# Performance work log

Measured on AMD Instinct MI355X. Metric: run time of the kernel, lower is better.

The kernel has to match this reference:

```python
import jax, jax.numpy as jnp
import numpy as np

EPS = 1e-8  # torch CosineSimilarity eps


def _l2_normalize(x):
    n = jnp.sqrt(jnp.sum(x * x, axis=-1, keepdims=True))
    return x / jnp.maximum(n, EPS)


def setup_inputs() -> dict:
    key = jax.random.key(0)
    k1, k2, k3 = jax.random.split(key, 3)
    B, D, K = 4096, 1024, 256
    datapoints = jax.random.normal(k1, (B, D), dtype=jnp.float32)
    centroid = jax.random.normal(k2, (K, D), dtype=jnp.float32)
    batch_cos_sim = jax.random.normal(k3, (B, B), dtype=jnp.float32)
    return {"datapoints": datapoints, "centroid": centroid, "batch_cos_sim": batch_cos_sim}


def reference(datapoints, centroid, batch_cos_sim):
    # --- _clustering: cosine similarity datapoints[B,D] vs centroid[K,D] (temp=1) ---
    dn = _l2_normalize(datapoints)                       # [B, D]
    cn = _l2_normalize(centroid)                         # [K, D]
    intra_cos_sim = jnp.einsum('bd,kd->bk', dn, cn)      # [B, K]
    dp_index = jnp.argmax(intra_cos_sim, axis=-1)        # [B]

    # --- _intra_class_adjacency: one-hot matmul, zero diagonal ---
    onehot = jax.nn.one_hot(dp_index, centroid.shape[0], dtype=jnp.float32)  # [B, K]
    dp_cluster = jnp.einsum('bk,ck->bc', onehot, onehot)                      # [B, B]
    B = datapoints.shape[0]
    dp_cluster = dp_cluster * (1.0 - jnp.eye(B, dtype=dp_cluster.dtype))
    index_dp = onehot.T.astype(jnp.int32)                # [K, B]

    # --- gather centroid each datapoint belongs to ---
    dp_centroid = centroid[dp_index]                     # [B, D]

    # --- provide_hard_negative: top-2, take 2nd-best centroid ---
    top_vals, top_idx = jax.lax.top_k(intra_cos_sim, 2)  # [B, 2]
    hard_neg_index = top_idx[:, 1]                       # [B]
    hard_negative = centroid[hard_neg_index]             # [B, D]

    return (intra_cos_sim, dp_index, dp_cluster, index_dp, dp_centroid,
            hard_negative, hard_neg_index, top_vals[:, 1])
```

## Files before the change

### kernel.cpp

```cpp
#include <hip/hip_runtime.h>
#include <hip/hip_bf16.h>
#include <math.h>

#define B_N 4096
#define D_N 1024
#define K_N 256
#define BK 32
#define NSTEP (D_N / BK)

typedef __attribute__((ext_vector_type(8))) short bf16x8;
typedef __attribute__((ext_vector_type(8))) unsigned short u16x8;
typedef __attribute__((ext_vector_type(4))) float f32x4;

static constexpr float K_EPS = 1e-8f;

static __device__ __forceinline__ unsigned short f32_to_bf16_rne(float f) {
    unsigned x = __builtin_bit_cast(unsigned, f);
    unsigned r = (x + 0x7FFFu + ((x >> 16) & 1u)) >> 16;
    return (unsigned short)r;
}
static __device__ __forceinline__ float bf16_bits_to_f32(unsigned short h) {
    unsigned x = ((unsigned)h) << 16;
    return __builtin_bit_cast(float, x);
}

__global__ __launch_bounds__(256) void kcent_kernel(
    const float* __restrict__ cent,
    ushort* __restrict__ phi, ushort* __restrict__ plo)
{
    int n   = blockIdx.x;
    int tid = threadIdx.x;
    float4 v = reinterpret_cast<const float4*>(cent + (size_t)n * D_N)[tid];
    float s = v.x * v.x + v.y * v.y + v.z * v.z + v.w * v.w;
    #pragma unroll
    for (int o = 32; o > 0; o >>= 1) s += __shfl_down(s, o);
    __shared__ float red[4];
    __shared__ float s_inv;
    if ((tid & 63) == 0) red[tid >> 6] = s;
    __syncthreads();
    if (tid == 0) {
        float t = red[0] + red[1] + red[2] + red[3];
        s_inv = 1.0f / fmaxf(sqrtf(t), K_EPS);
    }
    __syncthreads();
    float inv = s_inv;
    float e[4] = {v.x * inv, v.y * inv, v.z * inv, v.w * inv};
    ushort h4[4], l4[4];
    #pragma unroll
    for (int j = 0; j < 4; ++j) {
        ushort h = f32_to_bf16_rne(e[j]);
        float lo = e[j] - bf16_bits_to_f32(h);
        h4[j] = h;
        l4[j] = f32_to_bf16_rne(lo);
    }
    int nt = n >> 4, lr = n & 15;
    int k8 = tid >> 1, half = tid & 1;
    int t  = k8 >> 2, lg = k8 & 3;
    size_t chunk = (size_t)(nt * 32 + t) * 64 + lg * 16 + lr;
    *reinterpret_cast<ushort4*>(phi + chunk * 8 + half * 4) =
        make_ushort4(h4[0], h4[1], h4[2], h4[3]);
    *reinterpret_cast<ushort4*>(plo + chunk * 8 + half * 4) =
        make_ushort4(l4[0], l4[1], l4[2], l4[3]);
}

__global__ __launch_bounds__(512, 4) void kmain_kernel(
    const float* __restrict__ dp, const float* __restrict__ cent,
    const ushort* __restrict__ phi, const ushort* __restrict__ plo,
    float* __restrict__ out_sims, float* __restrict__ out_dpidx,
    float* __restrict__ out_hnidx, float* __restrict__ out_top1,
    float* __restrict__ out_dpcent, float* __restrict__ out_hneg,
    int* __restrict__ ws_dpidx)
{
    __shared__ ushort AhL[16 * 1024];
    __shared__ ushort AlL[16 * 1024];
    __shared__ float  simsL[16 * 256];
    int tid  = threadIdx.x;
    int lane = tid & 63;
    int w    = tid >> 6;
    int lr   = lane & 15;
    int lg   = lane >> 4;
    int brow = blockIdx.x * 16;

    {
        int grp = tid & 31;
        int row = tid >> 5;
        const float4* r4 = reinterpret_cast<const float4*>(
            dp + (size_t)(brow + row) * D_N);
        float s = 0.f;
        #pragma unroll
        for (int q = 0; q < 4; ++q) {
            float4 a = r4[grp * 2 + q * 64];
            float4 b = r4[grp * 2 + 1 + q * 64];
            s += a.x*a.x + a.y*a.y + a.z*a.z + a.w*a.w;
            s += b.x*b.x + b.y*b.y + b.z*b.z + b.w*b.w;
        }
        #pragma unroll
        for (int o = 1; o < 32; o <<= 1) s += __shfl_xor(s, o);
        float inv = 1.0f / fmaxf(sqrtf(s), K_EPS);
        asm volatile("" ::: "memory");
        #pragma unroll
        for (int q = 0; q < 4; ++q) {
            float4 a = r4[grp * 2 + q * 64];
            float4 b = r4[grp * 2 + 1 + q * 64];
            float e0 = a.x*inv, e1 = a.y*inv, e2 = a.z*inv, e3 = a.w*inv;
            float e4 = b.x*inv, e5 = b.y*inv, e6 = b.z*inv, e7 = b.w*inv;
            ushort h0=f32_to_bf16_rne(e0), h1=f32_to_bf16_rne(e1),
                   h2=f32_to_bf16_rne(e2), h3=f32_to_bf16_rne(e3),
                   h4=f32_to_bf16_rne(e4), h5=f32_to_bf16_rne(e5),
                   h6=f32_to_bf16_rne(e6), h7=f32_to_bf16_rne(e7);
            u16x8 hv = {h0,h1,h2,h3,h4,h5,h6,h7};
            u16x8 lv = {f32_to_bf16_rne(e0 - bf16_bits_to_f32(h0)),
                        f32_to_bf16_rne(e1 - bf16_bits_to_f32(h1)),
                        f32_to_bf16_rne(e2 - bf16_bits_to_f32(h2)),
                        f32_to_bf16_rne(e3 - bf16_bits_to_f32(h3)),
                        f32_to_bf16_rne(e4 - bf16_bits_to_f32(h4)),
                        f32_to_bf16_rne(e5 - bf16_bits_to_f32(h5)),
                        f32_to_bf16_rne(e6 - bf16_bits_to_f32(h6)),
                        f32_to_bf16_rne(e7 - bf16_bits_to_f32(h7))};
            int slot = (q * 32 + grp) ^ (row & 7);
            *reinterpret_cast<u16x8*>(&AhL[row * 1024 + slot * 8]) = hv;
            *reinterpret_cast<u16x8*>(&AlL[row * 1024 + slot * 8]) = lv;
        }
    }
    __syncthreads();

    const ushort* bh0 = phi + (size_t)w * 32768 + lane * 8;
    const ushort* bl0 = plo + (size_t)w * 32768 + lane * 8;
    const ushort* bh1 = bh0 + 16384;
    const ushort* bl1 = bl0 + 16384;

    f32x4 acc[2] = {};
    const char* AhC = (const char*)AhL;
    const char* AlC = (const char*)AlL;

    auto step = [&](int t, bf16x8 h0, bf16x8 l0, bf16x8 h1, bf16x8 l1) {
        int g = 4 * t + lg;
        unsigned ca = (unsigned)(g ^ (lr & 7));
        unsigned ao = (unsigned)lr * 2048u + ca * 16u;
        bf16x8 ah = *reinterpret_cast<const bf16x8*>(AhC + ao);
        bf16x8 al = *reinterpret_cast<const bf16x8*>(AlC + ao);
        acc[0] = __builtin_amdgcn_mfma_f32_16x16x32_bf16(ah, h0, acc[0], 0, 0, 0);
        acc[0] = __builtin_amdgcn_mfma_f32_16x16x32_bf16(ah, l0, acc[0], 0, 0, 0);
        acc[0] = __builtin_amdgcn_mfma_f32_16x16x32_bf16(al, h0, acc[0], 0, 0, 0);
        acc[1] = __builtin_amdgcn_mfma_f32_16x16x32_bf16(ah, h1, acc[1], 0, 0, 0);
        acc[1] = __builtin_amdgcn_mfma_f32_16x16x32_bf16(ah, l1, acc[1], 0, 0, 0);
        acc[1] = __builtin_amdgcn_mfma_f32_16x16x32_bf16(al, h1, acc[1], 0, 0, 0);
    };

    #define LB(t, H0, L0, H1, L1)                                        \
        H0 = *reinterpret_cast<const bf16x8*>(bh0 + (t) * 512);          \
        L0 = *reinterpret_cast<const bf16x8*>(bl0 + (t) * 512);          \
        H1 = *reinterpret_cast<const bf16x8*>(bh1 + (t) * 512);          \
        L1 = *reinterpret_cast<const bf16x8*>(bl1 + (t) * 512);

    bf16x8 ah0,al0,ah1,al1, bh0r,bl0r,bh1r,bl1r,
           ch0,cl0,ch1,cl1, dh0,dl0,dh1,dl1;
    LB(0, ah0, al0, ah1, al1)
    LB(1, bh0r, bl0r, bh1r, bl1r)
    LB(2, ch0, cl0, ch1, cl1)
    LB(3, dh0, dl0, dh1, dl1)
    #pragma unroll 1
    for (int t = 0; t < NSTEP; t += 4) {
        step(t + 0, ah0, al0, ah1, al1);
        if (t + 4 < NSTEP) { LB(t + 4, ah0, al0, ah1, al1) }
        step(t + 1, bh0r, bl0r, bh1r, bl1r);
        if (t + 5 < NSTEP) { LB(t + 5, bh0r, bl0r, bh1r, bl1r) }
        step(t + 2, ch0, cl0, ch1, cl1);
        if (t + 6 < NSTEP) { LB(t + 6, ch0, cl0, ch1, cl1) }
        step(t + 3, dh0, dl0, dh1, dl1);
        if (t + 7 < NSTEP) { LB(t + 7, dh0, dl0, dh1, dl1) }
    }
    #undef LB

    #pragma unroll
    for (int tt = 0; tt < 2; ++tt)
        #pragma unroll
        for (int r = 0; r < 4; ++r)
            simsL[(lg * 4 + r) * K_N + (w * 2 + tt) * 16 + lr] = acc[tt][r];
    __syncthreads();

    const float4* cent4 = reinterpret_cast<const float4*>(cent);
    #pragma unroll
    for (int rloc = 0; rloc < 2; ++rloc) {
        int row_l = w * 2 + rloc;
        int row   = brow + row_l;
        float4 c = *reinterpret_cast<const float4*>(&simsL[row_l * K_N + lane * 4]);
        *reinterpret_cast<float4*>(&out_sims[(size_t)row * K_N + lane * 4]) = c;
        float v1b = c.x; int i1 = lane * 4;
        float v2b = -INFINITY; int i2 = 0;
        {
            float vals[3] = {c.y, c.z, c.w};
            #pragma unroll
            for (int j = 0; j < 3; ++j) {
                float val = vals[j]; int idx = lane * 4 + j + 1;
                if (val > v1b) { v2b = v1b; i2 = i1; v1b = val; i1 = idx; }
                else if (val > v2b) { v2b = val; i2 = idx; }
            }
        }
        #pragma unroll
        for (int o = 1; o < 64; o <<= 1) {
            float ov1 = __shfl_xor(v1b, o);
            float ov2 = __shfl_xor(v2b, o);
            int   oi1 = __shfl_xor(i1, o);
            int   oi2 = __shfl_xor(i2, o);
            if (ov1 > v1b || (ov1 == v1b && oi1 < i1)) {
                float nv2; int ni2;
                if (v1b > ov2 || (v1b == ov2 && i1 < oi2)) { nv2 = v1b; ni2 = i1; }
                else { nv2 = ov2; ni2 = oi2; }
                v1b = ov1; i1 = oi1; v2b = nv2; i2 = ni2;
            } else if (ov1 > v2b || (ov1 == v2b && oi1 < i2)) {
                v2b = ov1; i2 = oi1;
            }
        }
        #pragma unroll
        for (int q = 0; q < 4; ++q) {
            float4 g1 = cent4[(size_t)i1 * 256 + q * 64 + lane];
            float4 g2 = cent4[(size_t)i2 * 256 + q * 64 + lane];
            reinterpret_cast<float4*>(out_dpcent + (size_t)row * D_N)[q * 64 + lane] = g1;
            reinterpret_cast<float4*>(out_hneg   + (size_t)row * D_N)[q * 64 + lane] = g2;
        }
        if (lane == 0) {
            out_dpidx[row] = (float)i1;
            out_hnidx[row] = (float)i2;
            out_top1[row]  = v2b;
            ws_dpidx[row]  = i1;
        }
    }
}

__global__ __launch_bounds__(256) void kclust_kernel(
    const int* __restrict__ dpidx,
    float* __restrict__ out_cluster, float* __restrict__ out_indexdp)
{
    int bid = blockIdx.x;
    int tid = threadIdx.x;
    const int4* dpi4 = reinterpret_cast<const int4*>(dpidx);
    if (bid < B_N) {
        int i = bid;
        int me = dpidx[i];
        float* dst = out_cluster + (size_t)i * B_N;
        #pragma unroll
        for (int q = 0; q < 4; ++q) {
            int j = q * 1024 + tid * 4;
            int4 ix = dpi4[j >> 2];
            float4 v;
            v.x = (ix.x == me && (j + 0) != i) ? 1.0f : 0.0f;
            v.y = (ix.y == me && (j + 1) != i) ? 1.0f : 0.0f;
            v.z = (ix.z == me && (j + 2) != i) ? 1.0f : 0.0f;
            v.w = (ix.w == me && (j + 3) != i) ? 1.0f : 0.0f;
            *reinterpret_cast<float4*>(dst + j) = v;
        }
    } else {
        int k = bid - B_N;
        float* dst = out_indexdp + (size_t)k * B_N;
        #pragma unroll
        for (int q = 0; q < 4; ++q) {
            int j = q * 1024 + tid * 4;
            int4 ix = dpi4[j >> 2];
            float4 v;
            v.x = (ix.x == k) ? 1.0f : 0.0f;
            v.y = (ix.y == k) ? 1.0f : 0.0f;
            v.z = (ix.z == k) ? 1.0f : 0.0f;
            v.w = (ix.w == k) ? 1.0f : 0.0f;
            *reinterpret_cast<float4*>(dst + j) = v;
        }
    }
}

extern "C" void kernel_launch(void* const* d_in, const int* in_sizes, int n_in,
                              void* d_out, int out_size, void* d_ws, size_t ws_size,
                              hipStream_t stream)
{
    const float* dp   = (const float*)d_in[0];
    const float* cent = (const float*)d_in[1];
    float* out = (float*)d_out;

    float* o_sims   = out;
    float* o_dpidx  = out + 1048576;
    float* o_clust  = out + 1052672;
    float* o_idxdp  = out + 17829888;
    float* o_dpcent = out + 18878464;
    float* o_hneg   = out + 23072768;
    float* o_hnidx  = out + 27267072;
    float* o_top1   = out + 27271168;

    char* ws = (char*)d_ws;
    ushort* phi  = (ushort*)ws;
    ushort* plo  = (ushort*)(ws + (512u << 10));
    int*    widx = (int*)(ws + (1u << 20));

    hipLaunchKernelGGL(kcent_kernel, dim3(K_N), dim3(256), 0, stream,
                       cent, phi, plo);
    hipLaunchKernelGGL(kmain_kernel, dim3(B_N / 16), dim3(512), 0, stream,
                       dp, cent, phi, plo,
                       o_sims, o_dpidx, o_hnidx, o_top1,
                       o_dpcent, o_hneg, widx);
    hipLaunchKernelGGL(kclust_kernel, dim3(B_N + K_N), dim3(256), 0, stream,
                       widx, o_clust, o_idxdp);
}
```

Baseline: 44.49 us.

## Use 1024-thread blocks with one N-tile per wave and deeper B prefetch

```diff
diff --git a/kernel.cpp b/kernel.cpp
--- a/kernel.cpp
+++ b/kernel.cpp
@@ -5,8 +5,7 @@
 #define B_N 4096
 #define D_N 1024
 #define K_N 256
-#define BK 32
-#define NSTEP (D_N / BK)
+#define NSTEP 32
 
 typedef __attribute__((ext_vector_type(8))) short bf16x8;
 typedef __attribute__((ext_vector_type(8))) unsigned short u16x8;
@@ -22,6 +21,24 @@
 static __device__ __forceinline__ float bf16_bits_to_f32(unsigned short h) {
     unsigned x = ((unsigned)h) << 16;
     return __builtin_bit_cast(float, x);
+}
+static __device__ __forceinline__ void cvt8(
+    float e0, float e1, float e2, float e3,
+    float e4, float e5, float e6, float e7, u16x8& hv, u16x8& lv)
+{
+    ushort h0=f32_to_bf16_rne(e0), h1=f32_to_bf16_rne(e1),
+           h2=f32_to_bf16_rne(e2), h3=f32_to_bf16_rne(e3),
+           h4=f32_to_bf16_rne(e4), h5=f32_to_bf16_rne(e5),
+           h6=f32_to_bf16_rne(e6), h7=f32_to_bf16_rne(e7);
+    hv = (u16x8){h0,h1,h2,h3,h4,h5,h6,h7};
+    lv = (u16x8){f32_to_bf16_rne(e0 - bf16_bits_to_f32(h0)),
+                 f32_to_bf16_rne(e1 - bf16_bits_to_f32(h1)),
+                 f32_to_bf16_rne(e2 - bf16_bits_to_f32(h2)),
+                 f32_to_bf16_rne(e3 - bf16_bits_to_f32(h3)),
+                 f32_to_bf16_rne(e4 - bf16_bits_to_f32(h4)),
+                 f32_to_bf16_rne(e5 - bf16_bits_to_f32(h5)),
+                 f32_to_bf16_rne(e6 - bf16_bits_to_f32(h6)),
+                 f32_to_bf16_rne(e7 - bf16_bits_to_f32(h7))};
 }
 
 __global__ __launch_bounds__(256) void kcent_kernel(
@@ -63,7 +80,7 @@
         make_ushort4(l4[0], l4[1], l4[2], l4[3]);
 }
 
-__global__ __launch_bounds__(512, 4) void kmain_kernel(
+__global__ __launch_bounds__(1024) void kmain_kernel(
     const float* __restrict__ dp, const float* __restrict__ cent,
     const ushort* __restrict__ phi, const ushort* __restrict__ plo,
     float* __restrict__ out_sims, float* __restrict__ out_dpidx,
@@ -81,110 +98,76 @@
     int lg   = lane >> 4;
     int brow = blockIdx.x * 16;
 
+    const ushort* bh = phi + (size_t)w * 32 * 512 + (size_t)lane * 8;
+    const ushort* bl = plo + (size_t)w * 32 * 512 + (size_t)lane * 8;
+
+    #define LBF(t, H, L)                                                  \
+        H = *reinterpret_cast<const bf16x8*>(bh + (size_t)(t) * 512);     \
+        L = *reinterpret_cast<const bf16x8*>(bl + (size_t)(t) * 512);
+
+    bf16x8 h0,l0,h1,l1,h2,l2,h3,l3,h4,l4,h5,l5,h6,l6,h7,l7;
+    LBF(0,h0,l0) LBF(1,h1,l1) LBF(2,h2,l2) LBF(3,h3,l3)
+    LBF(4,h4,l4) LBF(5,h5,l5) LBF(6,h6,l6) LBF(7,h7,l7)
+
     {
-        int grp = tid & 31;
-        int row = tid >> 5;
         const float4* r4 = reinterpret_cast<const float4*>(
-            dp + (size_t)(brow + row) * D_N);
-        float s = 0.f;
-        #pragma unroll
-        for (int q = 0; q < 4; ++q) {
-            float4 a = r4[grp * 2 + q * 64];
-            float4 b = r4[grp * 2 + 1 + q * 64];
-            s += a.x*a.x + a.y*a.y + a.z*a.z + a.w*a.w;
-            s += b.x*b.x + b.y*b.y + b.z*b.z + b.w*b.w;
-        }
-        #pragma unroll
-        for (int o = 1; o < 32; o <<= 1) s += __shfl_xor(s, o);
+            dp + (size_t)(brow + w) * D_N);
+        float4 a0 = r4[lane*4+0], a1 = r4[lane*4+1],
+               a2 = r4[lane*4+2], a3 = r4[lane*4+3];
+        float s = a0.x*a0.x + a0.y*a0.y + a0.z*a0.z + a0.w*a0.w
+                + a1.x*a1.x + a1.y*a1.y + a1.z*a1.z + a1.w*a1.w
+                + a2.x*a2.x + a2.y*a2.y + a2.z*a2.z + a2.w*a2.w
+                + a3.x*a3.x + a3.y*a3.y + a3.z*a3.z + a3.w*a3.w;
+        #pragma unroll
+        for (int o = 1; o < 64; o <<= 1) s += __shfl_xor(s, o);
         float inv = 1.0f / fmaxf(sqrtf(s), K_EPS);
-        asm volatile("" ::: "memory");
-        #pragma unroll
-        for (int q = 0; q < 4; ++q) {
-            float4 a = r4[grp * 2 + q * 64];
-            float4 b = r4[grp * 2 + 1 + q * 64];
-            float e0 = a.x*inv, e1 = a.y*inv, e2 = a.z*inv, e3 = a.w*inv;
-            float e4 = b.x*inv, e5 = b.y*inv, e6 = b.z*inv, e7 = b.w*inv;
-            ushort h0=f32_to_bf16_rne(e0), h1=f32_to_bf16_rne(e1),
-                   h2=f32_to_bf16_rne(e2), h3=f32_to_bf16_rne(e3),
-                   h4=f32_to_bf16_rne(e4), h5=f32_to_bf16_rne(e5),
-                   h6=f32_to_bf16_rne(e6), h7=f32_to_bf16_rne(e7);
-            u16x8 hv = {h0,h1,h2,h3,h4,h5,h6,h7};
-            u16x8 lv = {f32_to_bf16_rne(e0 - bf16_bits_to_f32(h0)),
-                        f32_to_bf16_rne(e1 - bf16_bits_to_f32(h1)),
-                        f32_to_bf16_rne(e2 - bf16_bits_to_f32(h2)),
-                        f32_to_bf16_rne(e3 - bf16_bits_to_f32(h3)),
-                        f32_to_bf16_rne(e4 - bf16_bits_to_f32(h4)),
-                        f32_to_bf16_rne(e5 - bf16_bits_to_f32(h5)),
-                        f32_to_bf16_rne(e6 - bf16_bits_to_f32(h6)),
-                        f32_to_bf16_rne(e7 - bf16_bits_to_f32(h7))};
-            int slot = (q * 32 + grp) ^ (row & 7);
-            *reinterpret_cast<u16x8*>(&AhL[row * 1024 + slot * 8]) = hv;
-            *reinterpret_cast<u16x8*>(&AlL[row * 1024 + slot * 8]) = lv;
-        }
-    }
-    __syncthreads();
-
-    const ushort* bh0 = phi + (size_t)w * 32768 + lane * 8;
-    const ushort* bl0 = plo + (size_t)w * 32768 + lane * 8;
-    const ushort* bh1 = bh0 + 16384;
-    const ushort* bl1 = bl0 + 16384;
-
-    f32x4 acc[2] = {};
+        u16x8 hv, lv;
+        cvt8(a0.x*inv, a0.y*inv, a0.z*inv, a0.w*inv,
+             a1.x*inv, a1.y*inv, a1.z*inv, a1.w*inv, hv, lv);
+        int slot = (lane*2 + 0) ^ (w & 7);
+        *reinterpret_cast<u16x8*>(&AhL[w*1024 + slot*8]) = hv;
+        *reinterpret_cast<u16x8*>(&AlL[w*1024 + slot*8]) = lv;
+        cvt8(a2.x*inv, a2.y*inv, a2.z*inv, a2.w*inv,
+             a3.x*inv, a3.y*inv, a3.z*inv, a3.w*inv, hv, lv);
+        slot = (lane*2 + 1) ^ (w & 7);
+        *reinterpret_cast<u16x8*>(&AhL[w*1024 + slot*8]) = hv;
+        *reinterpret_cast<u16x8*>(&AlL[w*1024 + slot*8]) = lv;
+    }
+    __syncthreads();
+
+    f32x4 acc = {};
     const char* AhC = (const char*)AhL;
     const char* AlC = (const char*)AlL;
-
-    auto step = [&](int t, bf16x8 h0, bf16x8 l0, bf16x8 h1, bf16x8 l1) {
-        int g = 4 * t + lg;
-        unsigned ca = (unsigned)(g ^ (lr & 7));
+    auto step = [&](int t, bf16x8 hb, bf16x8 lb) {
+        unsigned ca = (unsigned)((4*t + lg) ^ (lr & 7));
         unsigned ao = (unsigned)lr * 2048u + ca * 16u;
         bf16x8 ah = *reinterpret_cast<const bf16x8*>(AhC + ao);
         bf16x8 al = *reinterpret_cast<const bf16x8*>(AlC + ao);
-        acc[0] = __builtin_amdgcn_mfma_f32_16x16x32_bf16(ah, h0, acc[0], 0, 0, 0);
-        acc[0] = __builtin_amdgcn_mfma_f32_16x16x32_bf16(ah, l0, acc[0], 0, 0, 0);
-        acc[0] = __builtin_amdgcn_mfma_f32_16x16x32_bf16(al, h0, acc[0], 0, 0, 0);
-        acc[1] = __builtin_amdgcn_mfma_f32_16x16x32_bf16(ah, h1, acc[1], 0, 0, 0);
-        acc[1] = __builtin_amdgcn_mfma_f32_16x16x32_bf16(ah, l1, acc[1], 0, 0, 0);
-        acc[1] = __builtin_amdgcn_mfma_f32_16x16x32_bf16(al, h1, acc[1], 0, 0, 0);
+        acc = __builtin_amdgcn_mfma_f32_16x16x32_bf16(ah, hb, acc, 0, 0, 0);
+        acc = __builtin_amdgcn_mfma_f32_16x16x32_bf16(ah, lb, acc, 0, 0, 0);
+        acc = __builtin_amdgcn_mfma_f32_16x16x32_bf16(al, hb, acc, 0, 0, 0);
     };
-
-    #define LB(t, H0, L0, H1, L1)                                        \
-        H0 = *reinterpret_cast<const bf16x8*>(bh0 + (t) * 512);          \
-        L0 = *reinterpret_cast<const bf16x8*>(bl0 + (t) * 512);          \
-        H1 = *reinterpret_cast<const bf16x8*>(bh1 + (t) * 512);          \
-        L1 = *reinterpret_cast<const bf16x8*>(bl1 + (t) * 512);
-
-    bf16x8 ah0,al0,ah1,al1, bh0r,bl0r,bh1r,bl1r,
-           ch0,cl0,ch1,cl1, dh0,dl0,dh1,dl1;
-    LB(0, ah0, al0, ah1, al1)
-    LB(1, bh0r, bl0r, bh1r, bl1r)
-    LB(2, ch0, cl0, ch1, cl1)
-    LB(3, dh0, dl0, dh1, dl1)
     #pragma unroll 1
-    for (int t = 0; t < NSTEP; t += 4) {
-        step(t + 0, ah0, al0, ah1, al1);
-        if (t + 4 < NSTEP) { LB(t + 4, ah0, al0, ah1, al1) }
-        step(t + 1, bh0r, bl0r, bh1r, bl1r);
-        if (t + 5 < NSTEP) { LB(t + 5, bh0r, bl0r, bh1r, bl1r) }
-        step(t + 2, ch0, cl0, ch1, cl1);
-        if (t + 6 < NSTEP) { LB(t + 6, ch0, cl0, ch1, cl1) }
-        step(t + 3, dh0, dl0, dh1, dl1);
-        if (t + 7 < NSTEP) { LB(t + 7, dh0, dl0, dh1, dl1) }
-    }
-    #undef LB
+    for (int t = 0; t < NSTEP; t += 8) {
+        step(t + 0, h0, l0); if (t +  8 < NSTEP) { LBF(t +  8, h0, l0) }
+        step(t + 1, h1, l1); if (t +  9 < NSTEP) { LBF(t +  9, h1, l1) }
+        step(t + 2, h2, l2); if (t + 10 < NSTEP) { LBF(t + 10, h2, l2) }
+        step(t + 3, h3, l3); if (t + 11 < NSTEP) { LBF(t + 11, h3, l3) }
+        step(t + 4, h4, l4); if (t + 12 < NSTEP) { LBF(t + 12, h4, l4) }
+        step(t + 5, h5, l5); if (t + 13 < NSTEP) { LBF(t + 13, h5, l5) }
+        step(t + 6, h6, l6); if (t + 14 < NSTEP) { LBF(t + 14, h6, l6) }
+        step(t + 7, h7, l7); if (t + 15 < NSTEP) { LBF(t + 15, h7, l7) }
+    }
+    #undef LBF
 
     #pragma unroll
-    for (int tt = 0; tt < 2; ++tt)
-        #pragma unroll
-        for (int r = 0; r < 4; ++r)
-            simsL[(lg * 4 + r) * K_N + (w * 2 + tt) * 16 + lr] = acc[tt][r];
-    __syncthreads();
-
-    const float4* cent4 = reinterpret_cast<const float4*>(cent);
-    #pragma unroll
-    for (int rloc = 0; rloc < 2; ++rloc) {
-        int row_l = w * 2 + rloc;
-        int row   = brow + row_l;
-        float4 c = *reinterpret_cast<const float4*>(&simsL[row_l * K_N + lane * 4]);
+    for (int r = 0; r < 4; ++r)
+        simsL[(lg*4 + r) * K_N + w*16 + lr] = acc[r];
+    __syncthreads();
+
+    {
+        float4 c = *reinterpret_cast<const float4*>(&simsL[w * K_N + lane * 4]);
+        int row = brow + w;
         *reinterpret_cast<float4*>(&out_sims[(size_t)row * K_N + lane * 4]) = c;
         float v1b = c.x; int i1 = lane * 4;
         float v2b = -INFINITY; int i2 = 0;
@@ -212,12 +195,13 @@
                 v2b = ov1; i2 = oi1;
             }
         }
+        const float4* cent4 = reinterpret_cast<const float4*>(cent);
         #pragma unroll
         for (int q = 0; q < 4; ++q) {
             float4 g1 = cent4[(size_t)i1 * 256 + q * 64 + lane];
             float4 g2 = cent4[(size_t)i2 * 256 + q * 64 + lane];
-            reinterpret_cast<float4*>(out_dpcent + (size_t)row * D_N)[q * 64 + lane] = g1;
-            reinterpret_cast<float4*>(out_hneg   + (size_t)row * D_N)[q * 64 + lane] = g2;
+            reinterpret_cast<float4*>(out_dpcent + (size_t)row * D_N)[q*64 + lane] = g1;
+            reinterpret_cast<float4*>(out_hneg   + (size_t)row * D_N)[q*64 + lane] = g2;
         }
         if (lane == 0) {
             out_dpidx[row] = (float)i1;
@@ -291,7 +275,7 @@
 
     hipLaunchKernelGGL(kcent_kernel, dim3(K_N), dim3(256), 0, stream,
                        cent, phi, plo);
-    hipLaunchKernelGGL(kmain_kernel, dim3(B_N / 16), dim3(512), 0, stream,
+    hipLaunchKernelGGL(kmain_kernel, dim3(B_N / 16), dim3(1024), 0, stream,
                        dp, cent, phi, plo,
                        o_sims, o_dpidx, o_hnidx, o_top1,
                        o_dpcent, o_hneg, widx);
```

After: 44.06 us. Within noise of the previous version (-1.0%).
